# Optimization experiments

Hardware: AMD Instinct MI355X
Metric: run time of the kernel (lower is better)

## Reference

```python
import jax, jax.numpy as jnp
import numpy as np
import math

B, S, D, H = 4, 2048, 1024, 16
HD = D // H  # head dim = 64


def setup_inputs() -> dict:
    key = jax.random.key(0)
    ks = jax.random.split(key, 8)
    queries = jax.random.normal(ks[0], (B, S, D), dtype=jnp.float32)
    keys = jax.random.normal(ks[1], (B, S, D), dtype=jnp.float32)
    values = jax.random.normal(ks[2], (B, S, D), dtype=jnp.float32)
    valid_lens = jnp.maximum(jax.random.randint(ks[3], (B,), 0, S), 1).astype(jnp.int64)
    scale = 1.0 / math.sqrt(D)
    Wq = jax.random.normal(ks[4], (H, D, HD), dtype=jnp.float32) * scale
    Wk = jax.random.normal(ks[5], (H, D, HD), dtype=jnp.float32) * scale
    Wv = jax.random.normal(ks[6], (H, D, HD), dtype=jnp.float32) * scale
    Wo = jax.random.normal(ks[7], (H * HD, D), dtype=jnp.float32) * scale
    return {"queries": queries, "keys": keys, "values": values,
            "valid_lens": valid_lens, "Wq": Wq, "Wk": Wk, "Wv": Wv, "Wo": Wo}


def reference(queries, keys, values, valid_lens, Wq, Wk, Wv, Wo):
    # Per-head projections, batched over heads: [B,S,D] x [H,D,HD] -> [B,H,S,HD]
    q = jnp.einsum('bsd,hde->bhse', queries, Wq)
    k = jnp.einsum('bsd,hde->bhse', keys, Wk)
    v = jnp.einsum('bsd,hde->bhse', values, Wv)
    # Scaled dot-product scores: [B,H,S,S]
    scores = jnp.einsum('bhse,bhte->bhst', q, k) / jnp.sqrt(jnp.float32(HD))
    # Padding mask only (causal=False default in the torch forward)
    pad = jnp.arange(S)[None, :] >= valid_lens[:, None]  # [B,S] True = masked
    scores = jnp.where(pad[:, None, None, :], -jnp.inf, scores)
    attn = jax.nn.softmax(scores, axis=-1)
    out = jnp.einsum('bhst,bhte->bhse', attn, v)  # [B,H,S,HD]
    out = out.transpose(0, 2, 1, 3).reshape(q.shape[0], S, H * HD)  # concat heads
    return out @ Wo
```

## Files before the change

kernel.cpp:

```cpp
#include <hip/hip_runtime.h>
#include <hip/hip_bf16.h>

typedef __bf16 bf16;
typedef __attribute__((ext_vector_type(8))) __bf16 bf16x8;
typedef __attribute__((ext_vector_type(4))) float f32x4;

#define DEV __device__ __forceinline__

DEV float fexp2(float x) {
#if __has_builtin(__builtin_amdgcn_exp2f)
  return __builtin_amdgcn_exp2f(x);
#else
  return exp2f(x);
#endif
}

DEV void gload_lds16(const void* g, void* l) {
  __builtin_amdgcn_global_load_lds(
      (__attribute__((address_space(1))) void*)(g),
      (__attribute__((address_space(3))) void*)(l), 16, 0, 0);
}

template <int N>
DEV void waitvm() { asm volatile("s_waitcnt vmcnt(%0)" ::"n"(N) : "memory"); }
DEV void fence() { asm volatile("" ::: "memory"); }
DEV void bar() { fence(); __builtin_amdgcn_s_barrier(); fence(); }

__global__ void k_cvt_act(const float* __restrict__ q, const float* __restrict__ k,
                          const float* __restrict__ v, bf16* __restrict__ qb,
                          bf16* __restrict__ kb, bf16* __restrict__ vb) {
  const int bid = blockIdx.x;
  const int which = bid >> 12;
  const float* in = which == 0 ? q : which == 1 ? k : v;
  bf16* out = which == 0 ? qb : which == 1 ? kb : vb;
  const int i = (bid & 4095) * 256 + threadIdx.x;
  const float4* p = reinterpret_cast<const float4*>(in) + (size_t)i * 2;
  float4 a = p[0], b = p[1];
  bf16x8 o;
  o[0] = (bf16)a.x; o[1] = (bf16)a.y; o[2] = (bf16)a.z; o[3] = (bf16)a.w;
  o[4] = (bf16)b.x; o[5] = (bf16)b.y; o[6] = (bf16)b.z; o[7] = (bf16)b.w;
  *reinterpret_cast<bf16x8*>(out + (size_t)i * 8) = o;
}

__global__ void k_cvt_w(const float* __restrict__ Wq, const float* __restrict__ Wk,
                        const float* __restrict__ Wv, const float* __restrict__ Wo,
                        bf16* __restrict__ WqkvT, bf16* __restrict__ WoT) {
  const int idx = blockIdx.x * blockDim.x + threadIdx.x;
  const int which = idx >> 20, r = idx & ((1 << 20) - 1);
  if (which < 3) {
    const float* W = which == 0 ? Wq : which == 1 ? Wk : Wv;
    const int d = r & 1023, n = r >> 10;
    float val = W[((size_t)(n >> 6) << 16) + (size_t)d * 64 + (n & 63)];
    if (which == 0) val *= 0.180336880f;
    WqkvT[((size_t)which << 20) + r] = (bf16)val;
  } else {
    const int kk = r & 1023, n = r >> 10;
    WoT[r] = (bf16)Wo[(size_t)kk * 1024 + n];
  }
}

DEV void stageA(const bf16* __restrict__ Am, bf16 (*lds)[64], int k0, int tid) {
  const int wv = tid >> 6;
#pragma unroll
  for (int l = 0; l < 2; ++l) {
    const int row = l * 64 + (tid >> 3);
    const int e = (((tid & 7) ^ (row & 7)) << 3);
    gload_lds16(Am + (size_t)row * 1024 + k0 + e,
                (char*)lds + l * 8192 + wv * 1024);
  }
}
DEV void stageBh(const bf16* __restrict__ Bt, bf16 (*lds)[64], int h, int k0, int tid) {
  const int wv = tid >> 6;
#pragma unroll
  for (int l = 0; l < 2; ++l) {
    const int row = h * 128 + l * 64 + (tid >> 3);
    const int e = (((tid & 7) ^ (row & 7)) << 3);
    gload_lds16(Bt + (size_t)row * 1024 + k0 + e,
                (char*)lds + h * 16384 + l * 8192 + wv * 1024);
  }
}
DEV bf16x8 ldsfrag(const bf16 (*lds)[64], int row, int kk, int lgrp) {
  const int ch = ((kk << 2) + lgrp) ^ (row & 7);
  return *reinterpret_cast<const bf16x8*>((const char*)&lds[row][0] + (ch << 4));
}

#define GEMM_KLOOP(Am, Bt, acc)                                               \
  stageA(Am, AsB[0], 0, tid);                                                 \
  stageBh(Bt, BsB[0], 0, 0, tid);                                             \
  stageBh(Bt, BsB[0], 1, 0, tid);                                             \
  stageBh(Bt, BsB[1], 0, 64, tid);                                            \
  stageBh(Bt, BsB[1], 1, 64, tid);                                            \
  waitvm<4>();                                                                \
  bar();                                                                      \
  int cur = 0;                                                                \
  for (int kt = 0; kt < NT; ++kt) {                                           \
    bf16x8 bfr[4][2], afr[2][2];                                              \
    _Pragma("unroll") for (int n = 0; n < 4; ++n)                             \
        _Pragma("unroll") for (int kk = 0; kk < 2; ++kk)                      \
            bfr[n][kk] = ldsfrag(BsB[cur], wn * 64 + n * 16 + lid, kk, lgrp); \
    _Pragma("unroll") for (int mi = 0; mi < 2; ++mi)                          \
        _Pragma("unroll") for (int kk = 0; kk < 2; ++kk)                      \
            afr[mi][kk] = ldsfrag(AsB[cur], wr * 64 + mi * 16 + lid, kk, lgrp); \
    if (kt + 1 < NT) stageA(Am, AsB[cur ^ 1], (kt + 1) * 64, tid);            \
    bar();                                                                    \
    __builtin_amdgcn_s_setprio(1);                                            \
    _Pragma("unroll") for (int mi = 0; mi < 2; ++mi)                          \
        _Pragma("unroll") for (int n = 0; n < 4; ++n)                         \
            _Pragma("unroll") for (int kk = 0; kk < 2; ++kk)                  \
                acc[mi][n] = __builtin_amdgcn_mfma_f32_16x16x32_bf16(         \
                    afr[mi][kk], bfr[n][kk], acc[mi][n], 0, 0, 0);            \
    __builtin_amdgcn_s_setprio(0);                                            \
    bar();                                                                    \
    _Pragma("unroll") for (int mi = 0; mi < 2; ++mi)                          \
        _Pragma("unroll") for (int kk = 0; kk < 2; ++kk)                      \
            afr[mi][kk] = ldsfrag(AsB[cur], wr * 64 + (2 + mi) * 16 + lid, kk, lgrp); \
    if (kt + 2 < NT) {                                                        \
      stageBh(Bt, BsB[cur], 0, (kt + 2) * 64, tid);                           \
      stageBh(Bt, BsB[cur], 1, (kt + 2) * 64, tid);                           \
    }                                                                         \
    bar();                                                                    \
    __builtin_amdgcn_s_setprio(1);                                            \
    _Pragma("unroll") for (int mi = 0; mi < 2; ++mi)                          \
        _Pragma("unroll") for (int n = 0; n < 4; ++n)                         \
            _Pragma("unroll") for (int kk = 0; kk < 2; ++kk)                  \
                acc[2 + mi][n] = __builtin_amdgcn_mfma_f32_16x16x32_bf16(     \
                    afr[mi][kk], bfr[n][kk], acc[2 + mi][n], 0, 0, 0);        \
    __builtin_amdgcn_s_setprio(0);                                            \
    if (kt < NT - 2) waitvm<4>();                                             \
    else if (kt == NT - 2) waitvm<0>();                                       \
    bar();                                                                    \
    cur ^= 1;                                                                 \
  }

__global__ __launch_bounds__(512, 2) void k_gemm_qkv(const bf16* __restrict__ qA,
                                                     const bf16* __restrict__ kA,
                                                     const bf16* __restrict__ vA,
                                                     const bf16* __restrict__ Wt,
                                                     bf16* __restrict__ Qh,
                                                     bf16* __restrict__ Kh,
                                                     bf16* __restrict__ Vt) {
  __shared__ __align__(16) bf16 AsB[2][128][64];
  __shared__ __align__(16) bf16 BsB[2][256][64];
  const int tid = threadIdx.x, lane = tid & 63, w = tid >> 6;
  const int lgrp = lane >> 4, lid = lane & 15;
  const int wr = w >> 2, wn = w & 3;
  const int bid0 = blockIdx.x;
  const int bid = (bid0 & 7) * 96 + (bid0 >> 3);
  const int proj = bid >> 8;
  const int local = bid & 255;
  const int mt = local >> 2, ntl = local & 3;
  const int m0 = mt * 128, n0 = ntl * 256;
  const bf16* A = proj == 0 ? qA : proj == 1 ? kA : vA;
  const bf16* Am = A + (size_t)m0 * 1024;
  const bf16* Bt = Wt + ((size_t)proj * 1024 + n0) * 1024;

  f32x4 acc[4][4] = {};
  constexpr int NT = 16;
  GEMM_KLOOP(Am, Bt, acc)

  const int hh = (n0 >> 6) + wn;
  if (proj == 0) {
#pragma unroll
    for (int mm = 0; mm < 4; ++mm) {
      const int rowb = m0 + wr * 64 + mm * 16 + lgrp * 4;
      const int bb = rowb >> 11, s = rowb & 2047;
#pragma unroll
      for (int n = 0; n < 4; ++n) {
        const int e = n * 16 + lid;
        bf16* dst = Qh + (((size_t)bb * 16 + hh) * 2048 + s) * 64 + e;
#pragma unroll
        for (int r = 0; r < 4; ++r) dst[(size_t)r * 64] = (bf16)acc[mm][n][r];
      }
    }
  } else if (proj == 1) {
#pragma unroll
    for (int mm = 0; mm < 4; ++mm) {
      const int rowb = m0 + wr * 64 + mm * 16 + lgrp * 4;
      const int bb = rowb >> 11, s = rowb & 2047;
#pragma unroll
      for (int n = 0; n < 4; ++n) {
        const int e = n * 16 + lid;
#pragma unroll
        for (int r = 0; r < 4; ++r) {
          const int sr = s + r;
          Kh[(((size_t)bb * 16 + hh) * 2048 + sr) * 64 + (e ^ ((sr & 7) << 3))] =
              (bf16)acc[mm][n][r];
        }
      }
    }
  } else {
#pragma unroll
    for (int mm = 0; mm < 4; ++mm) {
      const int rowb = m0 + wr * 64 + mm * 16 + lgrp * 4;
      const int bb = rowb >> 11, s = rowb & 2047;
#pragma unroll
      for (int n = 0; n < 4; ++n) {
        const int e = n * 16 + lid;
        union { bf16 hv[4]; uint2 u; } tmp;
#pragma unroll
        for (int r = 0; r < 4; ++r) tmp.hv[r] = (bf16)acc[mm][n][r];
        bf16* dst = Vt + (((size_t)bb * 16 + hh) * 64 + e) * 2048 + (s ^ ((e & 7) << 3));
        *reinterpret_cast<uint2*>(dst) = tmp.u;
      }
    }
  }
}

__global__ __launch_bounds__(512, 2) void k_gemm_out8(const bf16* __restrict__ A,
                                                      const bf16* __restrict__ Wo,
                                                      float* __restrict__ C) {
  __shared__ __align__(16) bf16 AsB[2][128][64];
  __shared__ __align__(16) bf16 BsB[2][256][64];
  const int tid = threadIdx.x, lane = tid & 63, w = tid >> 6;
  const int lgrp = lane >> 4, lid = lane & 15;
  const int wr = w >> 2, wn = w & 3;
  const int bid0 = blockIdx.x;
  const int bid = (bid0 & 7) * 32 + (bid0 >> 3);
  const int mt = bid >> 2, ntl = bid & 3;
  const int m0 = mt * 128, n0 = ntl * 256;
  const bf16* Am = A + (size_t)m0 * 1024;
  const bf16* Bt = Wo + (size_t)n0 * 1024;

  f32x4 acc[4][4] = {};
  constexpr int NT = 16;
  GEMM_KLOOP(Am, Bt, acc)

#pragma unroll
  for (int mm = 0; mm < 4; ++mm) {
    const int rowb = m0 + wr * 64 + mm * 16 + lgrp * 4;
#pragma unroll
    for (int n = 0; n < 4; ++n) {
      const int col = n0 + wn * 64 + n * 16 + lid;
#pragma unroll
      for (int r = 0; r < 4; ++r)
        C[(size_t)(rowb + r) * 1024 + col] = acc[mm][n][r];
    }
  }
}

__global__ __launch_bounds__(256, 3) void k_flash(const bf16* __restrict__ Qh,
                                                  const bf16* __restrict__ Ksw,
                                                  const bf16* __restrict__ Vsw,
                                                  const int* __restrict__ valid,
                                                  bf16* __restrict__ Ob) {
  __shared__ __align__(16) char Ks[2][8192];
  __shared__ __align__(16) char Vs[2][8192];
  __shared__ __align__(16) char Plds[4][4096];
  const int tid = threadIdx.x, lane = tid & 63, w = tid >> 6;
  const int lgrp = lane >> 4, lid = lane & 15;
  const int blk = blockIdx.x;
  const int qt = blk & 15, bh = blk >> 4;
  const int b = bh >> 4, h = bh & 15;
  const int s0 = qt * 128 + w * 32;
  const bf16* Qp = Qh + ((size_t)bh * 2048 + s0) * 64;
  const bf16* Kp = Ksw + (size_t)bh * 2048 * 64;
  const bf16* Vp = Vsw + (size_t)bh * 64 * 2048;
  const int vl = valid[b];
  const int nt = (vl + 63) >> 6;
  const int full = vl >> 6;

  const int sr0 = 16 * w + (lane >> 3), col8 = (lane & 7) * 8;

  gload_lds16(Kp + (size_t)sr0 * 64 + col8, &Ks[0][(16 * w) * 128]);
  gload_lds16(Kp + (size_t)(sr0 + 8) * 64 + col8, &Ks[0][(16 * w + 8) * 128]);
  gload_lds16(Vp + (size_t)sr0 * 2048 + col8, &Vs[0][(16 * w) * 128]);
  gload_lds16(Vp + (size_t)(sr0 + 8) * 2048 + col8, &Vs[0][(16 * w + 8) * 128]);

  bf16x8 aq[2][2];
#pragma unroll
  for (int g = 0; g < 2; ++g)
#pragma unroll
    for (int c = 0; c < 2; ++c)
      aq[g][c] = *reinterpret_cast<const bf16x8*>(Qp + (g * 16 + lid) * 64 + c * 32 + lgrp * 8);

  f32x4 Of[2][4] = {};
  float mrow[2] = {-1e30f, -1e30f};
  float lpart[2] = {0.f, 0.f};
  char* Pw = &Plds[w][0];
  float* PwF = (float*)Pw;
  const int pswz = (lid & 7) << 4;

  int cur = 0;
  for (int t = 0; t < nt; ++t) {
    const int t0 = t * 64;
    __syncthreads();
    if (t + 1 < nt) {
      const int t1 = t0 + 64;
      gload_lds16(Kp + (size_t)(t1 + sr0) * 64 + col8, &Ks[cur ^ 1][(16 * w) * 128]);
      gload_lds16(Kp + (size_t)(t1 + sr0 + 8) * 64 + col8, &Ks[cur ^ 1][(16 * w + 8) * 128]);
      gload_lds16(Vp + (size_t)sr0 * 2048 + t1 + col8, &Vs[cur ^ 1][(16 * w) * 128]);
      gload_lds16(Vp + (size_t)(sr0 + 8) * 2048 + t1 + col8, &Vs[cur ^ 1][(16 * w + 8) * 128]);
    }
    f32x4 sc[2][4] = {{}, {}};
#pragma unroll
    for (int kk = 0; kk < 2; ++kk) {
      bf16x8 bkh[4];
#pragma unroll
      for (int ct = 0; ct < 4; ++ct) {
        const int row = ct * 16 + lid;
        bkh[ct] = *reinterpret_cast<const bf16x8*>(
            &Ks[cur][row * 128] + ((kk * 64 + lgrp * 16) ^ ((row & 7) << 4)));
      }
#pragma unroll
      for (int g = 0; g < 2; ++g)
#pragma unroll
        for (int ct = 0; ct < 4; ++ct)
          sc[g][ct] = __builtin_amdgcn_mfma_f32_16x16x32_bf16(bkh[ct], aq[g][kk],
                                                              sc[g][ct], 0, 0, 0);
    }
    if (t >= full) {
#pragma unroll
      for (int ct = 0; ct < 4; ++ct)
#pragma unroll
        for (int r = 0; r < 4; ++r) {
          const bool m = (t0 + ct * 16 + lgrp * 4 + r) >= vl;
          sc[0][ct][r] = m ? -1e30f : sc[0][ct][r];
          sc[1][ct][r] = m ? -1e30f : sc[1][ct][r];
        }
    }
    float vm[2];
#pragma unroll
    for (int g = 0; g < 2; ++g) {
      float v = fmaxf(fmaxf(fmaxf(sc[g][0][0], sc[g][0][1]), fmaxf(sc[g][0][2], sc[g][0][3])),
                      fmaxf(fmaxf(sc[g][1][0], sc[g][1][1]), fmaxf(sc[g][1][2], sc[g][1][3])));
      v = fmaxf(v, fmaxf(fmaxf(fmaxf(sc[g][2][0], sc[g][2][1]), fmaxf(sc[g][2][2], sc[g][2][3])),
                         fmaxf(fmaxf(sc[g][3][0], sc[g][3][1]), fmaxf(sc[g][3][2], sc[g][3][3]))));
      vm[g] = v;
    }
    if (__any((vm[0] > mrow[0] + 8.f) | (vm[1] > mrow[1] + 8.f))) {
#pragma unroll
      for (int g = 0; g < 2; ++g) {
        float v = vm[g];
        v = fmaxf(v, __shfl_xor(v, 16));
        v = fmaxf(v, __shfl_xor(v, 32));
        float mnew = fmaxf(mrow[g], v);
        float scl = fexp2(mrow[g] - mnew);
        mrow[g] = mnew;
        lpart[g] *= scl;
        if (lgrp == 0) PwF[g * 512 + lid] = scl;
      }
      asm volatile("s_waitcnt lgkmcnt(0)" ::: "memory");
      f32x4 sq0 = *reinterpret_cast<const f32x4*>(PwF + lgrp * 4);
      f32x4 sq1 = *reinterpret_cast<const f32x4*>(PwF + 512 + lgrp * 4);
#pragma unroll
      for (int f = 0; f < 4; ++f)
#pragma unroll
        for (int r = 0; r < 4; ++r) {
          Of[0][f][r] *= sq0[r];
          Of[1][f][r] *= sq1[r];
        }
    }
#pragma unroll
    for (int g = 0; g < 2; ++g)
#pragma unroll
      for (int ct = 0; ct < 4; ++ct)
#pragma unroll
        for (int r = 0; r < 4; ++r)
          sc[g][ct][r] = fexp2(sc[g][ct][r] - mrow[g]);
#pragma unroll
    for (int g = 0; g < 2; ++g)
#pragma unroll
      for (int ct = 0; ct < 4; ++ct) {
        union { bf16 hv[2]; unsigned int u; } p0, p1;
        p0.hv[0] = (bf16)sc[g][ct][0]; p0.hv[1] = (bf16)sc[g][ct][1];
        p1.hv[0] = (bf16)sc[g][ct][2]; p1.hv[1] = (bf16)sc[g][ct][3];
        char* base = Pw + g * 2048 + lid * 128 + ((ct * 32 + lgrp * 8) ^ pswz);
        *reinterpret_cast<unsigned int*>(base) = p0.u;
        *reinterpret_cast<unsigned int*>(base + 4) = p1.u;
      }
    asm volatile("s_waitcnt lgkmcnt(0)" ::: "memory");
    bf16x8 pa[2][2];
#pragma unroll
    for (int g = 0; g < 2; ++g) {
      pa[g][0] = *reinterpret_cast<const bf16x8*>(Pw + g * 2048 + lid * 128 + ((lgrp * 16) ^ pswz));
      pa[g][1] = *reinterpret_cast<const bf16x8*>(Pw + g * 2048 + lid * 128 + ((64 + lgrp * 16) ^ pswz));
    }
#pragma unroll
    for (int f = 0; f < 4; ++f) {
      const int row = f * 16 + lid;
      const char* vb = &Vs[cur][row * 128];
      const int msk = (row & 7) << 4;
      bf16x8 bv0 = *reinterpret_cast<const bf16x8*>(vb + ((lgrp * 16) ^ msk));
      bf16x8 bv1 = *reinterpret_cast<const bf16x8*>(vb + ((64 + lgrp * 16) ^ msk));
      Of[0][f] = __builtin_amdgcn_mfma_f32_16x16x32_bf16(pa[0][0], bv0, Of[0][f], 0, 0, 0);
      Of[0][f] = __builtin_amdgcn_mfma_f32_16x16x32_bf16(pa[0][1], bv1, Of[0][f], 0, 0, 0);
      Of[1][f] = __builtin_amdgcn_mfma_f32_16x16x32_bf16(pa[1][0], bv0, Of[1][f], 0, 0, 0);
      Of[1][f] = __builtin_amdgcn_mfma_f32_16x16x32_bf16(pa[1][1], bv1, Of[1][f], 0, 0, 0);
    }
#pragma unroll
    for (int g = 0; g < 2; ++g)
      lpart[g] += ((sc[g][0][0] + sc[g][0][1]) + (sc[g][0][2] + sc[g][0][3])) +
                  ((sc[g][1][0] + sc[g][1][1]) + (sc[g][1][2] + sc[g][1][3])) +
                  ((sc[g][2][0] + sc[g][2][1]) + (sc[g][2][2] + sc[g][2][3])) +
                  ((sc[g][3][0] + sc[g][3][1]) + (sc[g][3][2] + sc[g][3][3]));
    cur ^= 1;
  }
#pragma unroll
  for (int g = 0; g < 2; ++g) {
    float l = lpart[g];
    l += __shfl_xor(l, 16);
    l += __shfl_xor(l, 32);
    if (lgrp == 0) PwF[g * 512 + lid] = 1.f / l;
  }
  asm volatile("s_waitcnt lgkmcnt(0)" ::: "memory");
  f32x4 iq0 = *reinterpret_cast<const f32x4*>(PwF + lgrp * 4);
  f32x4 iq1 = *reinterpret_cast<const f32x4*>(PwF + 512 + lgrp * 4);
  bf16* Op = Ob + ((size_t)b * 2048 + s0) * 1024 + h * 64;
#pragma unroll
  for (int r = 0; r < 4; ++r)
#pragma unroll
    for (int f = 0; f < 4; ++f) {
      Op[(size_t)(lgrp * 4 + r) * 1024 + f * 16 + lid] = (bf16)(Of[0][f][r] * iq0[r]);
      Op[(size_t)(16 + lgrp * 4 + r) * 1024 + f * 16 + lid] = (bf16)(Of[1][f][r] * iq1[r]);
    }
}

extern "C" void kernel_launch(void* const* d_in, const int* in_sizes, int n_in,
                              void* d_out, int out_size, void* d_ws, size_t ws_size,
                              hipStream_t stream) {
  const float* q = (const float*)d_in[0];
  const float* k = (const float*)d_in[1];
  const float* v = (const float*)d_in[2];
  const int* vl = (const int*)d_in[3];
  const float* Wq = (const float*)d_in[4];
  const float* Wk = (const float*)d_in[5];
  const float* Wv = (const float*)d_in[6];
  const float* Wo = (const float*)d_in[7];

  char* ws = (char*)d_ws;
  const size_t SZW = (size_t)1024 * 1024 * 2;
  const size_t SZT = (size_t)8192 * 1024 * 2;
  bf16* WqkvT = (bf16*)(ws);
  bf16* WoT = (bf16*)(ws + 3 * SZW);
  bf16* Qh  = (bf16*)(ws + 4 * SZW);
  bf16* Kh  = (bf16*)(ws + 4 * SZW + SZT);
  bf16* Vt  = (bf16*)(ws + 4 * SZW + 2 * SZT);
  bf16* qb  = (bf16*)(ws + 4 * SZW + 3 * SZT);
  bf16* kb  = (bf16*)(ws + 4 * SZW + 4 * SZT);
  bf16* vb  = (bf16*)(ws + 4 * SZW + 5 * SZT);
  bf16* attnb = qb;

  k_cvt_act<<<12288, 256, 0, stream>>>(q, k, v, qb, kb, vb);
  k_cvt_w<<<16384, 256, 0, stream>>>(Wq, Wk, Wv, Wo, WqkvT, WoT);
  k_gemm_qkv<<<768, 512, 0, stream>>>(qb, kb, vb, WqkvT, Qh, Kh, Vt);
  k_flash<<<1024, 256, 0, stream>>>(Qh, Kh, Vt, vl, attnb);
  k_gemm_out8<<<256, 512, 0, stream>>>(attnb, WoT, (float*)d_out);
}
```

Baseline: 181.4 us.

## Fuse fp32-to-bf16 activation conversion into QKV projection GEMM

Removes the separate activation conversion kernel. The QKV GEMM now loads fp32 activations straight into registers, converts them to bf16 and writes them swizzled into LDS, with the next K tile's loads overlapped with the MFMA work. This avoids writing and re-reading about 48 MB of intermediate bf16 activations and saves one kernel launch. In exchange each block loads twice as many A bytes from global memory (re-read across the 4 N tiles), needs extra registers and extra lgkm waits, and the A path no longer uses direct-to-LDS loads.

```diff
diff --git a/kernel.cpp b/kernel.cpp
--- a/kernel.cpp
+++ b/kernel.cpp
@@ -23,24 +23,9 @@
 
 template <int N>
 DEV void waitvm() { asm volatile("s_waitcnt vmcnt(%0)" ::"n"(N) : "memory"); }
+DEV void waitlgkm0() { asm volatile("s_waitcnt lgkmcnt(0)" ::: "memory"); }
 DEV void fence() { asm volatile("" ::: "memory"); }
 DEV void bar() { fence(); __builtin_amdgcn_s_barrier(); fence(); }
-
-__global__ void k_cvt_act(const float* __restrict__ q, const float* __restrict__ k,
-                          const float* __restrict__ v, bf16* __restrict__ qb,
-                          bf16* __restrict__ kb, bf16* __restrict__ vb) {
-  const int bid = blockIdx.x;
-  const int which = bid >> 12;
-  const float* in = which == 0 ? q : which == 1 ? k : v;
-  bf16* out = which == 0 ? qb : which == 1 ? kb : vb;
-  const int i = (bid & 4095) * 256 + threadIdx.x;
-  const float4* p = reinterpret_cast<const float4*>(in) + (size_t)i * 2;
-  float4 a = p[0], b = p[1];
-  bf16x8 o;
-  o[0] = (bf16)a.x; o[1] = (bf16)a.y; o[2] = (bf16)a.z; o[3] = (bf16)a.w;
-  o[4] = (bf16)b.x; o[5] = (bf16)b.y; o[6] = (bf16)b.z; o[7] = (bf16)b.w;
-  *reinterpret_cast<bf16x8*>(out + (size_t)i * 8) = o;
-}
 
 __global__ void k_cvt_w(const float* __restrict__ Wq, const float* __restrict__ Wk,
                         const float* __restrict__ Wv, const float* __restrict__ Wo,
@@ -82,6 +67,28 @@
 DEV bf16x8 ldsfrag(const bf16 (*lds)[64], int row, int kk, int lgrp) {
   const int ch = ((kk << 2) + lgrp) ^ (row & 7);
   return *reinterpret_cast<const bf16x8*>((const char*)&lds[row][0] + (ch << 4));
+}
+
+DEV void loadA_f32(const float* __restrict__ Am, int k0, int tid, float4 v[4]) {
+#pragma unroll
+  for (int l = 0; l < 2; ++l) {
+    const int row = l * 64 + (tid >> 3);
+    const float* src = Am + (size_t)row * 1024 + k0 + (tid & 7) * 8;
+    v[l * 2] = *reinterpret_cast<const float4*>(src);
+    v[l * 2 + 1] = *reinterpret_cast<const float4*>(src + 4);
+  }
+}
+DEV void writeA_lds(bf16 (*lds)[64], int tid, const float4 v[4]) {
+#pragma unroll
+  for (int l = 0; l < 2; ++l) {
+    const int row = l * 64 + (tid >> 3);
+    const int ch = (tid & 7) ^ (row & 7);
+    union { bf16 h[8]; bf16x8 v8; } u;
+    const float* f = (const float*)&v[l * 2];
+#pragma unroll
+    for (int j = 0; j < 8; ++j) u.h[j] = (bf16)f[j];
+    *reinterpret_cast<bf16x8*>((char*)&lds[row][0] + (ch << 4)) = u.v8;
+  }
 }
 
 #define GEMM_KLOOP(Am, Bt, acc)                                               \
@@ -132,9 +139,9 @@
     cur ^= 1;                                                                 \
   }
 
-__global__ __launch_bounds__(512, 2) void k_gemm_qkv(const bf16* __restrict__ qA,
-                                                     const bf16* __restrict__ kA,
-                                                     const bf16* __restrict__ vA,
+__global__ __launch_bounds__(512, 2) void k_gemm_qkv(const float* __restrict__ qF,
+                                                     const float* __restrict__ kF,
+                                                     const float* __restrict__ vF,
                                                      const bf16* __restrict__ Wt,
                                                      bf16* __restrict__ Qh,
                                                      bf16* __restrict__ Kh,
@@ -150,13 +157,80 @@
   const int local = bid & 255;
   const int mt = local >> 2, ntl = local & 3;
   const int m0 = mt * 128, n0 = ntl * 256;
-  const bf16* A = proj == 0 ? qA : proj == 1 ? kA : vA;
-  const bf16* Am = A + (size_t)m0 * 1024;
+  const float* A = proj == 0 ? qF : proj == 1 ? kF : vF;
+  const float* Am = A + (size_t)m0 * 1024;
   const bf16* Bt = Wt + ((size_t)proj * 1024 + n0) * 1024;
 
   f32x4 acc[4][4] = {};
   constexpr int NT = 16;
-  GEMM_KLOOP(Am, Bt, acc)
+
+  float4 areg[4];
+  loadA_f32(Am, 0, tid, areg);
+  stageBh(Bt, BsB[0], 0, 0, tid);
+  stageBh(Bt, BsB[0], 1, 0, tid);
+  stageBh(Bt, BsB[1], 0, 64, tid);
+  stageBh(Bt, BsB[1], 1, 64, tid);
+  waitvm<8>();
+  writeA_lds(AsB[0], tid, areg);
+  waitvm<4>();
+  waitlgkm0();
+  bar();
+
+  int cur = 0;
+  for (int kt = 0; kt < NT; ++kt) {
+    bf16x8 bfr[4][2], afr[2][2];
+#pragma unroll
+    for (int n = 0; n < 4; ++n)
+#pragma unroll
+      for (int kk = 0; kk < 2; ++kk)
+        bfr[n][kk] = ldsfrag(BsB[cur], wn * 64 + n * 16 + lid, kk, lgrp);
+#pragma unroll
+    for (int mi = 0; mi < 2; ++mi)
+#pragma unroll
+      for (int kk = 0; kk < 2; ++kk)
+        afr[mi][kk] = ldsfrag(AsB[cur], wr * 64 + mi * 16 + lid, kk, lgrp);
+    if (kt + 1 < NT) loadA_f32(Am, (kt + 1) * 64, tid, areg);
+    bar();
+    __builtin_amdgcn_s_setprio(1);
+#pragma unroll
+    for (int mi = 0; mi < 2; ++mi)
+#pragma unroll
+      for (int n = 0; n < 4; ++n)
+#pragma unroll
+        for (int kk = 0; kk < 2; ++kk)
+          acc[mi][n] = __builtin_amdgcn_mfma_f32_16x16x32_bf16(
+              afr[mi][kk], bfr[n][kk], acc[mi][n], 0, 0, 0);
+    __builtin_amdgcn_s_setprio(0);
+    bar();
+#pragma unroll
+    for (int mi = 0; mi < 2; ++mi)
+#pragma unroll
+      for (int kk = 0; kk < 2; ++kk)
+        afr[mi][kk] = ldsfrag(AsB[cur], wr * 64 + (2 + mi) * 16 + lid, kk, lgrp);
+    if (kt + 2 < NT) {
+      stageBh(Bt, BsB[cur], 0, (kt + 2) * 64, tid);
+      stageBh(Bt, BsB[cur], 1, (kt + 2) * 64, tid);
+    }
+    if (kt + 1 < NT) {
+      if (kt + 2 < NT) waitvm<4>();
+      else waitvm<0>();
+      writeA_lds(AsB[cur ^ 1], tid, areg);
+    }
+    bar();
+    __builtin_amdgcn_s_setprio(1);
+#pragma unroll
+    for (int mi = 0; mi < 2; ++mi)
+#pragma unroll
+      for (int n = 0; n < 4; ++n)
+#pragma unroll
+        for (int kk = 0; kk < 2; ++kk)
+          acc[2 + mi][n] = __builtin_amdgcn_mfma_f32_16x16x32_bf16(
+              afr[mi][kk], bfr[n][kk], acc[2 + mi][n], 0, 0, 0);
+    __builtin_amdgcn_s_setprio(0);
+    waitlgkm0();
+    bar();
+    cur ^= 1;
+  }
 
   const int hh = (n0 >> 6) + wn;
   if (proj == 0) {
@@ -435,14 +509,10 @@
   bf16* Qh  = (bf16*)(ws + 4 * SZW);
   bf16* Kh  = (bf16*)(ws + 4 * SZW + SZT);
   bf16* Vt  = (bf16*)(ws + 4 * SZW + 2 * SZT);
-  bf16* qb  = (bf16*)(ws + 4 * SZW + 3 * SZT);
-  bf16* kb  = (bf16*)(ws + 4 * SZW + 4 * SZT);
-  bf16* vb  = (bf16*)(ws + 4 * SZW + 5 * SZT);
-  bf16* attnb = qb;
-
-  k_cvt_act<<<12288, 256, 0, stream>>>(q, k, v, qb, kb, vb);
+  bf16* attnb = (bf16*)(ws + 4 * SZW + 3 * SZT);
+
   k_cvt_w<<<16384, 256, 0, stream>>>(Wq, Wk, Wv, Wo, WqkvT, WoT);
-  k_gemm_qkv<<<768, 512, 0, stream>>>(qb, kb, vb, WqkvT, Qh, Kh, Vt);
+  k_gemm_qkv<<<768, 512, 0, stream>>>(q, k, v, WqkvT, Qh, Kh, Vt);
   k_flash<<<1024, 256, 0, stream>>>(Qh, Kh, Vt, vl, attnb);
   k_gemm_out8<<<256, 512, 0, stream>>>(attnb, WoT, (float*)d_out);
 }
```

New measurement: 192.9 us. 1.06x slower.
